# Optimization experiments

Measured on AMD Instinct MI355X. Metric: run time of the kernel, lower is better.

The kernel has to match this reference:

```python
import jax, jax.numpy as jnp
import numpy as np

N, C, H, E = 100000, 128, 8, 600000
HD = C // H
EPS = 1e-5


def _layernorm(x, g, b):
    mu = jnp.mean(x, axis=-1, keepdims=True)
    var = jnp.var(x, axis=-1, keepdims=True)
    return (x - mu) * jax.lax.rsqrt(var + EPS) * g + b


def setup_inputs() -> dict:
    key = jax.random.key(0)
    ks = jax.random.split(key, 12)
    s = 1.0 / np.sqrt(C)
    x = jax.random.normal(ks[0], (N, C), dtype=jnp.float32)
    edge_index = jax.random.randint(ks[1], (2, E), 0, N, dtype=jnp.int64)
    # linear weights stored [in, out]
    Wq = jax.random.normal(ks[2], (C, C), jnp.float32) * s
    Wk = jax.random.normal(ks[3], (C, C), jnp.float32) * s
    Wv = jax.random.normal(ks[4], (C, C), jnp.float32) * s
    Wo = jax.random.normal(ks[5], (C, C), jnp.float32) * s
    W1 = jax.random.normal(ks[6], (C, 4 * C), jnp.float32) * s
    W2 = jax.random.normal(ks[7], (4 * C, C), jnp.float32) * (1.0 / np.sqrt(4 * C))
    return {
        'x': x, 'edge_index': edge_index,
        'Wq': Wq, 'bq': jnp.zeros((C,), jnp.float32),
        'Wk': Wk, 'bk': jnp.zeros((C,), jnp.float32),
        'Wv': Wv, 'bv': jnp.zeros((C,), jnp.float32),
        'Wo': Wo, 'bo': jnp.zeros((C,), jnp.float32),
        'W1': W1, 'b1': jnp.zeros((4 * C,), jnp.float32),
        'W2': W2, 'b2': jnp.zeros((C,), jnp.float32),
        'g1': jnp.ones((C,), jnp.float32), 'beta1': jnp.zeros((C,), jnp.float32),
        'g2': jnp.ones((C,), jnp.float32), 'beta2': jnp.zeros((C,), jnp.float32),
    }


def reference(x, edge_index, Wq, bq, Wk, bk, Wv, bv, Wo, bo,
              W1, b1, W2, b2, g1, beta1, g2, beta2):
    src = edge_index[0]  # x_j (source nodes)
    dst = edge_index[1]  # x_i (target nodes, aggregation index)

    residual = x
    h = _layernorm(x, g1, beta1)

    # project at node level, then gather per edge (same math as per-edge proj)
    Q = h @ Wq + bq  # [N, C]
    K = h @ Wk + bk
    V = h @ Wv + bv

    q = Q[dst].reshape(E, H, HD)
    k = K[src].reshape(E, H, HD)
    v = V[src].reshape(E, H, HD)

    attn = jnp.sum(q * k, axis=-1) / np.sqrt(HD)  # [E, H]
    attn = jax.nn.softmax(attn, axis=-1)          # softmax over heads (per source)
    msg = (v * attn[..., None]).reshape(E, C)     # [E, C]

    aggr = jax.ops.segment_sum(msg, dst, num_segments=N)  # [N, C]
    out = aggr @ Wo + bo
    x = out + residual

    residual = x
    h = _layernorm(x, g2, beta2)
    h = jax.nn.relu(h @ W1 + b1) @ W2 + b2
    return h + residual
```

## Files before the change

### kernel.cpp

```cpp
#include <hip/hip_runtime.h>
#include <hip/hip_bf16.h>

#define C_DIM 128
#define EPS_LN 1e-5f

typedef short bf16x8 __attribute__((ext_vector_type(8)));
typedef float f32x4  __attribute__((ext_vector_type(4)));
typedef __hip_bfloat16 bf16;

__device__ inline unsigned short f2bu(float f) {
    bf16 h = __float2bfloat16(f);
    return *reinterpret_cast<unsigned short*>(&h);
}
__device__ inline float blo(unsigned int u) { return __uint_as_float(u << 16); }
__device__ inline float bhi(unsigned int u) { return __uint_as_float(u & 0xffff0000u); }
__device__ inline ushort4 pack4(float a, float b, float c, float d) {
    ushort4 r; r.x = f2bu(a); r.y = f2bu(b); r.z = f2bu(c); r.w = f2bu(d); return r;
}

__device__ inline void async_copy16(const bf16* g, bf16* s) {
    __builtin_amdgcn_global_load_lds(
        (const __attribute__((address_space(1))) unsigned int*)g,
        (__attribute__((address_space(3))) unsigned int*)s,
        16, 0, 0);
}

__global__ __launch_bounds__(256) void wconv_all(
    const float* __restrict__ Wq, const float* __restrict__ Wk,
    const float* __restrict__ Wv, const float* __restrict__ Wo,
    const float* __restrict__ W1, const float* __restrict__ W2,
    const float* __restrict__ bq, const float* __restrict__ bk,
    const float* __restrict__ bv, bf16* __restrict__ dst) {
    int idx = blockIdx.x * 256 + threadIdx.x;
    if (idx < 65536) {
        int r = idx >> 14, o = idx & 16383;
        int k = o >> 7, nn = o & 127;
        const float* W = (r == 0) ? Wq : (r == 1) ? Wk : (r == 2) ? Wv : Wo;
        dst[(r << 14) + nn * 128 + k] = __float2bfloat16(W[o]);
    } else if (idx < 131072) {
        int o = idx - 65536;
        int k = o >> 9, nn = o & 511;
        dst[65536 + nn * 128 + k] = __float2bfloat16(W1[o]);
    } else if (idx < 196608) {
        int o = idx - 131072;
        int k = o >> 7, nn = o & 127;
        dst[131072 + nn * 512 + k] = __float2bfloat16(W2[o]);
    } else if (idx < 196992) {
        int j = idx - 196608;
        int grp = j >> 7, col = j & 127;
        const float* bp = (grp == 0) ? bq : (grp == 1) ? bk : bv;
        ((float*)(dst + 196608))[j] = bp[col];
    }
}

__global__ __launch_bounds__(256) void zeroi_kernel(int* __restrict__ p, int n) {
    int i = blockIdx.x * 256 + threadIdx.x;
    if (i < n) p[i] = 0;
}

__global__ __launch_bounds__(256) void ln_kernel(
    const float* __restrict__ x, const float* __restrict__ g,
    const float* __restrict__ b, bf16* __restrict__ out, int n) {
    int wave = threadIdx.x >> 6;
    int lane = threadIdx.x & 63;
    int row = blockIdx.x * 4 + wave;
    if (row >= n) return;
    float2 v = ((const float2*)(x + (size_t)row * C_DIM))[lane];
    float s  = v.x + v.y;
    float ss = v.x * v.x + v.y * v.y;
    #pragma unroll
    for (int o = 1; o < 64; o <<= 1) {
        s  += __shfl_xor(s, o);
        ss += __shfl_xor(ss, o);
    }
    float mu  = s * (1.0f / C_DIM);
    float var = ss * (1.0f / C_DIM) - mu * mu;
    float rs  = rsqrtf(var + EPS_LN);
    float2 gg = ((const float2*)g)[lane];
    float2 bb = ((const float2*)b)[lane];
    __hip_bfloat162 o2;
    o2.x = __float2bfloat16((v.x - mu) * rs * gg.x + bb.x);
    o2.y = __float2bfloat16((v.y - mu) * rs * gg.y + bb.y);
    ((__hip_bfloat162*)(out + (size_t)row * C_DIM))[lane] = o2;
}

template<bool OUTBF16, bool RELU, bool FUSE_LN, int KSTEPS>
__global__ __launch_bounds__(256) void gemm_lds(
    const bf16* __restrict__ A, int lda,
    const bf16* __restrict__ Bt, int Kfull,
    const float* __restrict__ biasBase,
    void* __restrict__ Cd, int ldc, size_t obStride,
    const float* __restrict__ resid, int ldres,
    int M,
    const float* __restrict__ g, const float* __restrict__ be,
    bf16* __restrict__ h2) {
    __shared__ bf16 As[128][128];
    __shared__ bf16 Bs[128][128];
    int tid  = threadIdx.x;
    int lane = tid & 63;
    int w    = tid >> 6;
    int m = lane & 15, q = lane >> 4;
    int row0 = blockIdx.x * 128;
    const bf16* Bbase = Bt + (size_t)blockIdx.y * 128 * Kfull;

    f32x4 acc[2][8];
    #pragma unroll
    for (int rt = 0; rt < 2; rt++)
        #pragma unroll
        for (int ct = 0; ct < 8; ct++) acc[rt][ct] = (f32x4){0.f, 0.f, 0.f, 0.f};

    int rsub  = lane >> 4;
    int cslot = lane & 15;

    for (int kt = 0; kt < KSTEPS; kt++) {
        #pragma unroll
        for (int i = 0; i < 8; i++) {
            int arow = w * 32 + i * 4 + rsub;
            int scol = (cslot ^ (arow & 7)) << 3;
            int garow = row0 + arow;
            if (garow > M - 1) garow = M - 1;
            async_copy16(A + (size_t)garow * lda + kt * 128 + scol, &As[w * 32 + i * 4][0]);
            async_copy16(Bbase + (size_t)arow * Kfull + kt * 128 + scol, &Bs[w * 32 + i * 4][0]);
        }
        __syncthreads();
        #pragma unroll
        for (int ks = 0; ks < 4; ks++) {
            int sofs = ((ks * 4 + q) ^ (m & 7)) << 3;
            bf16x8 af0 = *(const bf16x8*)&As[w * 32 + m][sofs];
            bf16x8 af1 = *(const bf16x8*)&As[w * 32 + 16 + m][sofs];
            #pragma unroll
            for (int ct = 0; ct < 8; ct++) {
                bf16x8 bf = *(const bf16x8*)&Bs[ct * 16 + m][sofs];
                acc[0][ct] = __builtin_amdgcn_mfma_f32_16x16x32_bf16(bf, af0, acc[0][ct], 0, 0, 0);
                acc[1][ct] = __builtin_amdgcn_mfma_f32_16x16x32_bf16(bf, af1, acc[1][ct], 0, 0, 0);
            }
        }
        if (kt + 1 < KSTEPS) __syncthreads();
    }

    #pragma unroll
    for (int rt = 0; rt < 2; rt++) {
        int row = row0 + w * 32 + rt * 16 + m;
        bool valid = row < M;
        float vals[8][4];
        #pragma unroll
        for (int ct = 0; ct < 8; ct++) {
            int col = ct * 16 + q * 4;
            float4 bv = make_float4(0.f, 0.f, 0.f, 0.f);
            if (biasBase) bv = *(const float4*)(biasBase + blockIdx.y * 128 + col);
            float4 rv = make_float4(0.f, 0.f, 0.f, 0.f);
            if (resid && valid) rv = *(const float4*)(resid + (size_t)row * ldres + col);
            vals[ct][0] = acc[rt][ct][0] + bv.x + rv.x;
            vals[ct][1] = acc[rt][ct][1] + bv.y + rv.y;
            vals[ct][2] = acc[rt][ct][2] + bv.z + rv.z;
            vals[ct][3] = acc[rt][ct][3] + bv.w + rv.w;
        }
        if (FUSE_LN) {
            float s1 = 0.f, s2 = 0.f;
            #pragma unroll
            for (int ct = 0; ct < 8; ct++)
                #pragma unroll
                for (int r = 0; r < 4; r++) { s1 += vals[ct][r]; s2 += vals[ct][r] * vals[ct][r]; }
            s1 += __shfl_xor(s1, 16); s1 += __shfl_xor(s1, 32);
            s2 += __shfl_xor(s2, 16); s2 += __shfl_xor(s2, 32);
            float mu  = s1 * (1.0f / 128.f);
            float var = s2 * (1.0f / 128.f) - mu * mu;
            float rs  = rsqrtf(var + EPS_LN);
            if (valid) {
                #pragma unroll
                for (int ct = 0; ct < 8; ct++) {
                    int col = ct * 16 + q * 4;
                    *(float4*)((float*)Cd + (size_t)row * ldc + col) =
                        make_float4(vals[ct][0], vals[ct][1], vals[ct][2], vals[ct][3]);
                    float4 gg = *(const float4*)(g + col);
                    float4 bb = *(const float4*)(be + col);
                    *(ushort4*)(h2 + (size_t)row * 128 + col) =
                        pack4((vals[ct][0] - mu) * rs * gg.x + bb.x,
                              (vals[ct][1] - mu) * rs * gg.y + bb.y,
                              (vals[ct][2] - mu) * rs * gg.z + bb.z,
                              (vals[ct][3] - mu) * rs * gg.w + bb.w);
                }
            }
        } else if (valid) {
            #pragma unroll
            for (int ct = 0; ct < 8; ct++) {
                int col = ct * 16 + q * 4;
                float v0 = vals[ct][0], v1 = vals[ct][1];
                float v2 = vals[ct][2], v3 = vals[ct][3];
                if (RELU) {
                    v0 = fmaxf(v0, 0.f); v1 = fmaxf(v1, 0.f);
                    v2 = fmaxf(v2, 0.f); v3 = fmaxf(v3, 0.f);
                }
                if (OUTBF16) {
                    *(ushort4*)((bf16*)Cd + blockIdx.y * obStride + (size_t)row * ldc + col) =
                        pack4(v0, v1, v2, v3);
                } else {
                    *(float4*)((float*)Cd + blockIdx.y * obStride + (size_t)row * ldc + col) =
                        make_float4(v0, v1, v2, v3);
                }
            }
        }
    }
}

__device__ inline float dot8(uint4 a, uint4 b) {
    return blo(a.x) * blo(b.x) + bhi(a.x) * bhi(b.x)
         + blo(a.y) * blo(b.y) + bhi(a.y) * bhi(b.y)
         + blo(a.z) * blo(b.z) + bhi(a.z) * bhi(b.z)
         + blo(a.w) * blo(b.w) + bhi(a.w) * bhi(b.w);
}

__global__ __launch_bounds__(256) void attn_kernel(
    const bf16* __restrict__ Q, const bf16* __restrict__ K,
    const int* __restrict__ eidx, float* __restrict__ attn, int E_) {
    int gw = blockIdx.x * 4 + (threadIdx.x >> 6);
    int lane = threadIdx.x & 63;
    int e = gw * 8 + (lane >> 3);
    int h = lane & 7;
    bool v = e < E_;
    int src = v ? eidx[e] : 0;
    int dst = v ? eidx[E_ + e] : 0;
    const uint4* qp = (const uint4*)(Q + (size_t)dst * 128 + h * 16);
    const uint4* kp = (const uint4*)(K + (size_t)src * 128 + h * 16);
    uint4 q0 = qp[0], q1 = qp[1];
    uint4 k0 = kp[0], k1 = kp[1];
    float s = (dot8(q0, k0) + dot8(q1, k1)) * 0.25f;
    float mx = s;
    mx = fmaxf(mx, __shfl_xor(mx, 1));
    mx = fmaxf(mx, __shfl_xor(mx, 2));
    mx = fmaxf(mx, __shfl_xor(mx, 4));
    float ex = expf(s - mx);
    float sum = ex;
    sum += __shfl_xor(sum, 1);
    sum += __shfl_xor(sum, 2);
    sum += __shfl_xor(sum, 4);
    if (v) attn[(size_t)e * 8 + h] = ex / sum;
}

__global__ __launch_bounds__(256) void hist_kernel(
    const int* __restrict__ eidx, int* __restrict__ deg, int E_) {
    int e = blockIdx.x * 256 + threadIdx.x;
    if (e >= E_) return;
    atomicAdd(&deg[eidx[E_ + e]], 1);
}

__global__ __launch_bounds__(256) void alloc_kernel(
    const int* __restrict__ deg, int* __restrict__ start,
    int* __restrict__ cursor, int* __restrict__ counter, int n) {
    int i = blockIdx.x * 256 + threadIdx.x;
    if (i >= n) return;
    int d = deg[i];
    int s = atomicAdd(counter, d);
    start[i] = s;
    cursor[i] = s;
}

__global__ __launch_bounds__(256) void scatter_kernel(
    const int* __restrict__ eidx, int* __restrict__ cursor,
    int2* __restrict__ edata, int E_) {
    int e = blockIdx.x * 256 + threadIdx.x;
    if (e >= E_) return;
    int src = eidx[e];
    int dst = eidx[E_ + e];
    int pos = atomicAdd(&cursor[dst], 1);
    edata[pos] = make_int2(src, e);
}

__global__ __launch_bounds__(256) void aggr_kernel(
    const bf16* __restrict__ V, const float* __restrict__ attnW,
    const int* __restrict__ start, const int* __restrict__ deg,
    const int2* __restrict__ edata, bf16* __restrict__ ag, int n) {
    int wave = threadIdx.x >> 6;
    int lane = threadIdx.x & 63;
    int i = blockIdx.x * 4 + wave;
    if (i >= n) return;
    int s = start[i], d = deg[i];
    int h = lane >> 3;
    float ax = 0.f, ay = 0.f, bx = 0.f, by = 0.f;
    int j = s, e_ = s + d;
    for (; j + 2 <= e_; j += 2) {
        int2 e0 = edata[j], e1 = edata[j + 1];
        float a0 = attnW[(size_t)e0.y * 8 + h];
        float a1 = attnW[(size_t)e1.y * 8 + h];
        unsigned u0 = ((const unsigned*)(V + (size_t)e0.x * 128))[lane];
        unsigned u1 = ((const unsigned*)(V + (size_t)e1.x * 128))[lane];
        ax += a0 * blo(u0); ay += a0 * bhi(u0);
        bx += a1 * blo(u1); by += a1 * bhi(u1);
    }
    if (j < e_) {
        int2 e0 = edata[j];
        float a0 = attnW[(size_t)e0.y * 8 + h];
        unsigned u0 = ((const unsigned*)(V + (size_t)e0.x * 128))[lane];
        ax += a0 * blo(u0); ay += a0 * bhi(u0);
    }
    ax += bx; ay += by;
    __hip_bfloat162 o2;
    o2.x = __float2bfloat16(ax);
    o2.y = __float2bfloat16(ay);
    ((__hip_bfloat162*)(ag + (size_t)i * 128))[lane] = o2;
}

extern "C" void kernel_launch(void* const* d_in, const int* in_sizes, int n_in,
                              void* d_out, int out_size, void* d_ws, size_t ws_size,
                              hipStream_t stream) {
    const float* x   = (const float*)d_in[0];
    const int*  eidx = (const int*)d_in[1];
    const float* Wq = (const float*)d_in[2];  const float* bq = (const float*)d_in[3];
    const float* Wk = (const float*)d_in[4];  const float* bk = (const float*)d_in[5];
    const float* Wv = (const float*)d_in[6];  const float* bv = (const float*)d_in[7];
    const float* Wo = (const float*)d_in[8];  const float* bo = (const float*)d_in[9];
    const float* W1 = (const float*)d_in[10]; const float* b1 = (const float*)d_in[11];
    const float* W2 = (const float*)d_in[12]; const float* b2 = (const float*)d_in[13];
    const float* g1 = (const float*)d_in[14]; const float* be1 = (const float*)d_in[15];
    const float* g2 = (const float*)d_in[16]; const float* be2 = (const float*)d_in[17];
    float* out = (float*)d_out;

    int n  = in_sizes[0] / C_DIM;
    int E_ = in_sizes[1] / 2;
    size_t nf = (size_t)n * 128;

    bf16* Wt    = (bf16*)d_ws;
    float* bqkv = (float*)(Wt + 196608);
    bf16* reg0  = (bf16*)(bqkv + 384);
    bf16* h1 = reg0;
    bf16* Qb = reg0 + nf;
    bf16* Kb = reg0 + 2 * nf;
    bf16* Vb = reg0 + 3 * nf;
    bf16* uB = reg0;
    bf16* ag = reg0 + 4 * nf;
    char* r2 = (char*)(ag + nf);
    float* attnW = (float*)r2;
    int2* edata  = (int2*)(attnW + (size_t)E_ * 8);
    int*  ideg   = (int*)(edata + E_);
    int*  counter = ideg + n;
    int*  istart  = ideg + n + 1;
    int*  icursor = istart + n;
    bf16* h2 = (bf16*)r2;

    dim3 b256(256);
    dim3 lnGrid((n + 3) / 4);
    int rb = (n + 127) / 128;
    dim3 eGrid8((E_ + 31) / 32);
    dim3 eGrid((E_ + 255) / 256);
    dim3 nGrid((n + 255) / 256);
    dim3 n1Grid((n + 1 + 255) / 256);
    dim3 n4Grid((n + 3) / 4);

    wconv_all<<<dim3(770), b256, 0, stream>>>(Wq, Wk, Wv, Wo, W1, W2, bq, bk, bv, Wt);
    zeroi_kernel<<<n1Grid, b256, 0, stream>>>(ideg, n + 1);
    ln_kernel<<<lnGrid, b256, 0, stream>>>(x, g1, be1, h1, n);
    gemm_lds<true, false, false, 1><<<dim3(rb, 3), b256, 0, stream>>>(
        h1, 128, Wt, 128, bqkv, Qb, 128, nf, nullptr, 0, n, nullptr, nullptr, nullptr);
    attn_kernel<<<eGrid8, b256, 0, stream>>>(Qb, Kb, eidx, attnW, E_);
    hist_kernel<<<eGrid, b256, 0, stream>>>(eidx, ideg, E_);
    alloc_kernel<<<nGrid, b256, 0, stream>>>(ideg, istart, icursor, counter, n);
    scatter_kernel<<<eGrid, b256, 0, stream>>>(eidx, icursor, edata, E_);
    aggr_kernel<<<n4Grid, b256, 0, stream>>>(Vb, attnW, istart, ideg, edata, ag, n);
    gemm_lds<false, false, true, 1><<<dim3(rb, 1), b256, 0, stream>>>(
        ag, 128, Wt + 49152, 128, bo, out, 128, 0, x, 128, n, g2, be2, h2);
    gemm_lds<true, true, false, 1><<<dim3(rb, 4), b256, 0, stream>>>(
        h2, 128, Wt + 65536, 128, b1, uB, 512, 128, nullptr, 0, n, nullptr, nullptr, nullptr);
    gemm_lds<false, false, false, 4><<<dim3(rb, 1), b256, 0, stream>>>(
        uB, 512, Wt + 131072, 512, b2, out, 128, 0, out, 128, n, nullptr, nullptr, nullptr);
}
```

Baseline: 481.4 us.

## Fuse edge attention scoring into CSR aggregation kernel

Removes the separate per-edge attention kernel and its float attention-weight buffer. The aggregation kernel now loads each destination node's Q row once and, for every incoming edge, gathers the K row alongside the V row. It computes the per-head dot products and the softmax over heads with wave shuffles, then accumulates the weighted V. This drops the attention-weight writes and reads and the stored edge id, at the cost of an extra K gather and a longer shuffle chain inside the aggregation loop.

```diff
diff --git a/kernel.cpp b/kernel.cpp
--- a/kernel.cpp
+++ b/kernel.cpp
@@ -203,40 +203,6 @@
     }
 }
 
-__device__ inline float dot8(uint4 a, uint4 b) {
-    return blo(a.x) * blo(b.x) + bhi(a.x) * bhi(b.x)
-         + blo(a.y) * blo(b.y) + bhi(a.y) * bhi(b.y)
-         + blo(a.z) * blo(b.z) + bhi(a.z) * bhi(b.z)
-         + blo(a.w) * blo(b.w) + bhi(a.w) * bhi(b.w);
-}
-
-__global__ __launch_bounds__(256) void attn_kernel(
-    const bf16* __restrict__ Q, const bf16* __restrict__ K,
-    const int* __restrict__ eidx, float* __restrict__ attn, int E_) {
-    int gw = blockIdx.x * 4 + (threadIdx.x >> 6);
-    int lane = threadIdx.x & 63;
-    int e = gw * 8 + (lane >> 3);
-    int h = lane & 7;
-    bool v = e < E_;
-    int src = v ? eidx[e] : 0;
-    int dst = v ? eidx[E_ + e] : 0;
-    const uint4* qp = (const uint4*)(Q + (size_t)dst * 128 + h * 16);
-    const uint4* kp = (const uint4*)(K + (size_t)src * 128 + h * 16);
-    uint4 q0 = qp[0], q1 = qp[1];
-    uint4 k0 = kp[0], k1 = kp[1];
-    float s = (dot8(q0, k0) + dot8(q1, k1)) * 0.25f;
-    float mx = s;
-    mx = fmaxf(mx, __shfl_xor(mx, 1));
-    mx = fmaxf(mx, __shfl_xor(mx, 2));
-    mx = fmaxf(mx, __shfl_xor(mx, 4));
-    float ex = expf(s - mx);
-    float sum = ex;
-    sum += __shfl_xor(sum, 1);
-    sum += __shfl_xor(sum, 2);
-    sum += __shfl_xor(sum, 4);
-    if (v) attn[(size_t)e * 8 + h] = ex / sum;
-}
-
 __global__ __launch_bounds__(256) void hist_kernel(
     const int* __restrict__ eidx, int* __restrict__ deg, int E_) {
     int e = blockIdx.x * 256 + threadIdx.x;
@@ -257,43 +223,74 @@
 
 __global__ __launch_bounds__(256) void scatter_kernel(
     const int* __restrict__ eidx, int* __restrict__ cursor,
-    int2* __restrict__ edata, int E_) {
+    int* __restrict__ esrc, int E_) {
     int e = blockIdx.x * 256 + threadIdx.x;
     if (e >= E_) return;
     int src = eidx[e];
     int dst = eidx[E_ + e];
     int pos = atomicAdd(&cursor[dst], 1);
-    edata[pos] = make_int2(src, e);
-}
-
-__global__ __launch_bounds__(256) void aggr_kernel(
-    const bf16* __restrict__ V, const float* __restrict__ attnW,
+    esrc[pos] = src;
+}
+
+__global__ __launch_bounds__(256) void attn_aggr_kernel(
+    const bf16* __restrict__ Q, const bf16* __restrict__ K,
+    const bf16* __restrict__ V,
     const int* __restrict__ start, const int* __restrict__ deg,
-    const int2* __restrict__ edata, bf16* __restrict__ ag, int n) {
+    const int* __restrict__ esrc, bf16* __restrict__ ag, int n) {
     int wave = threadIdx.x >> 6;
     int lane = threadIdx.x & 63;
     int i = blockIdx.x * 4 + wave;
     if (i >= n) return;
     int s = start[i], d = deg[i];
-    int h = lane >> 3;
-    float ax = 0.f, ay = 0.f, bx = 0.f, by = 0.f;
+    unsigned qu = ((const unsigned*)(Q + (size_t)i * 128))[lane];
+    float qx = blo(qu), qy = bhi(qu);
+    float ax = 0.f, ay = 0.f;
     int j = s, e_ = s + d;
     for (; j + 2 <= e_; j += 2) {
-        int2 e0 = edata[j], e1 = edata[j + 1];
-        float a0 = attnW[(size_t)e0.y * 8 + h];
-        float a1 = attnW[(size_t)e1.y * 8 + h];
-        unsigned u0 = ((const unsigned*)(V + (size_t)e0.x * 128))[lane];
-        unsigned u1 = ((const unsigned*)(V + (size_t)e1.x * 128))[lane];
-        ax += a0 * blo(u0); ay += a0 * bhi(u0);
-        bx += a1 * blo(u1); by += a1 * bhi(u1);
+        int s0 = esrc[j], s1 = esrc[j + 1];
+        unsigned k0 = ((const unsigned*)(K + (size_t)s0 * 128))[lane];
+        unsigned k1 = ((const unsigned*)(K + (size_t)s1 * 128))[lane];
+        unsigned v0 = ((const unsigned*)(V + (size_t)s0 * 128))[lane];
+        unsigned v1 = ((const unsigned*)(V + (size_t)s1 * 128))[lane];
+        float p0 = qx * blo(k0) + qy * bhi(k0);
+        float p1 = qx * blo(k1) + qy * bhi(k1);
+        p0 += __shfl_xor(p0, 1); p1 += __shfl_xor(p1, 1);
+        p0 += __shfl_xor(p0, 2); p1 += __shfl_xor(p1, 2);
+        p0 += __shfl_xor(p0, 4); p1 += __shfl_xor(p1, 4);
+        p0 *= 0.25f; p1 *= 0.25f;
+        float m0 = fmaxf(p0, __shfl_xor(p0, 8));
+        float m1 = fmaxf(p1, __shfl_xor(p1, 8));
+        m0 = fmaxf(m0, __shfl_xor(m0, 16)); m1 = fmaxf(m1, __shfl_xor(m1, 16));
+        m0 = fmaxf(m0, __shfl_xor(m0, 32)); m1 = fmaxf(m1, __shfl_xor(m1, 32));
+        float e0 = expf(p0 - m0), e1 = expf(p1 - m1);
+        float t0 = e0 + __shfl_xor(e0, 8);
+        float t1 = e1 + __shfl_xor(e1, 8);
+        t0 += __shfl_xor(t0, 16); t1 += __shfl_xor(t1, 16);
+        t0 += __shfl_xor(t0, 32); t1 += __shfl_xor(t1, 32);
+        float a0 = e0 / t0, a1 = e1 / t1;
+        ax += a0 * blo(v0) + a1 * blo(v1);
+        ay += a0 * bhi(v0) + a1 * bhi(v1);
     }
     if (j < e_) {
-        int2 e0 = edata[j];
-        float a0 = attnW[(size_t)e0.y * 8 + h];
-        unsigned u0 = ((const unsigned*)(V + (size_t)e0.x * 128))[lane];
-        ax += a0 * blo(u0); ay += a0 * bhi(u0);
-    }
-    ax += bx; ay += by;
+        int s0 = esrc[j];
+        unsigned k0 = ((const unsigned*)(K + (size_t)s0 * 128))[lane];
+        unsigned v0 = ((const unsigned*)(V + (size_t)s0 * 128))[lane];
+        float p0 = qx * blo(k0) + qy * bhi(k0);
+        p0 += __shfl_xor(p0, 1);
+        p0 += __shfl_xor(p0, 2);
+        p0 += __shfl_xor(p0, 4);
+        p0 *= 0.25f;
+        float m0 = fmaxf(p0, __shfl_xor(p0, 8));
+        m0 = fmaxf(m0, __shfl_xor(m0, 16));
+        m0 = fmaxf(m0, __shfl_xor(m0, 32));
+        float e0 = expf(p0 - m0);
+        float t0 = e0 + __shfl_xor(e0, 8);
+        t0 += __shfl_xor(t0, 16);
+        t0 += __shfl_xor(t0, 32);
+        float a0 = e0 / t0;
+        ax += a0 * blo(v0);
+        ay += a0 * bhi(v0);
+    }
     __hip_bfloat162 o2;
     o2.x = __float2bfloat16(ax);
     o2.y = __float2bfloat16(ay);
@@ -329,9 +326,8 @@
     bf16* uB = reg0;
     bf16* ag = reg0 + 4 * nf;
     char* r2 = (char*)(ag + nf);
-    float* attnW = (float*)r2;
-    int2* edata  = (int2*)(attnW + (size_t)E_ * 8);
-    int*  ideg   = (int*)(edata + E_);
+    int*  esrc   = (int*)r2;
+    int*  ideg   = esrc + E_;
     int*  counter = ideg + n;
     int*  istart  = ideg + n + 1;
     int*  icursor = istart + n;
@@ -340,7 +336,6 @@
     dim3 b256(256);
     dim3 lnGrid((n + 3) / 4);
     int rb = (n + 127) / 128;
-    dim3 eGrid8((E_ + 31) / 32);
     dim3 eGrid((E_ + 255) / 256);
     dim3 nGrid((n + 255) / 256);
     dim3 n1Grid((n + 1 + 255) / 256);
@@ -351,11 +346,10 @@
     ln_kernel<<<lnGrid, b256, 0, stream>>>(x, g1, be1, h1, n);
     gemm_lds<true, false, false, 1><<<dim3(rb, 3), b256, 0, stream>>>(
         h1, 128, Wt, 128, bqkv, Qb, 128, nf, nullptr, 0, n, nullptr, nullptr, nullptr);
-    attn_kernel<<<eGrid8, b256, 0, stream>>>(Qb, Kb, eidx, attnW, E_);
     hist_kernel<<<eGrid, b256, 0, stream>>>(eidx, ideg, E_);
     alloc_kernel<<<nGrid, b256, 0, stream>>>(ideg, istart, icursor, counter, n);
-    scatter_kernel<<<eGrid, b256, 0, stream>>>(eidx, icursor, edata, E_);
-    aggr_kernel<<<n4Grid, b256, 0, stream>>>(Vb, attnW, istart, ideg, edata, ag, n);
+    scatter_kernel<<<eGrid, b256, 0, stream>>>(eidx, icursor, esrc, E_);
+    attn_aggr_kernel<<<n4Grid, b256, 0, stream>>>(Qb, Kb, Vb, istart, ideg, esrc, ag, n);
     gemm_lds<false, false, true, 1><<<dim3(rb, 1), b256, 0, stream>>>(
         ag, 128, Wt + 49152, 128, bo, out, 128, 0, x, 128, n, g2, be2, h2);
     gemm_lds<true, true, false, 1><<<dim3(rb, 4), b256, 0, stream>>>(
```

Measured after the change: 468.0 us. -2.8%, faster.
